# Kernel optimization log

Measured on AMD Instinct MI355X. Metric: run time of the kernel, lower is better.

## Reference

```python
import jax, jax.numpy as jnp
import numpy as np

KS = 3
N = KS ** 3  # 27 kernel taps
EPS = 1e-5

def conv3d(x, w, stride=1, padding=0):
    return jax.lax.conv_general_dilated(
        x, w, (stride,) * 3, [(padding, padding)] * 3,
        dimension_numbers=('NCDHW', 'OIDHW', 'NCDHW'))

def batchnorm(x, gamma, beta):
    mu = jnp.mean(x, axis=(0, 2, 3, 4), keepdims=True)
    var = jnp.var(x, axis=(0, 2, 3, 4), keepdims=True)
    return (x - mu) * jax.lax.rsqrt(var + EPS) * gamma[None, :, None, None, None] + beta[None, :, None, None, None]

def deform_conv3d(x, w_p, b_p, w_m, b_m, w_dc):
    b, c, D, H, W = x.shape
    offset = conv3d(x, w_p, padding=1) + b_p[None, :, None, None, None]      # (b,3N,D,H,W)
    m = jax.nn.sigmoid(conv3d(x, w_m, padding=1) + b_m[None, :, None, None, None])  # (b,N,D,H,W)
    x_pad = jnp.pad(x, ((0, 0), (0, 0), (1, 1), (1, 1), (1, 1)))
    Dp, Hp, Wp = D + 2, H + 2, W + 2
    r = jnp.arange(-(KS - 1) // 2, KS // 2 + 1, dtype=x.dtype)
    pn_d, pn_h, pn_w = [a.reshape(-1) for a in jnp.meshgrid(r, r, r, indexing='ij')]
    off = offset.transpose(0, 2, 3, 4, 1)                                    # (b,D,H,W,3N)
    p0_d = jnp.arange(1, D + 1, dtype=x.dtype)[:, None, None, None]
    p0_h = jnp.arange(1, H + 1, dtype=x.dtype)[None, :, None, None]
    p0_w = jnp.arange(1, W + 1, dtype=x.dtype)[None, None, :, None]
    pd = p0_d + pn_d + off[..., :N]
    ph = p0_h + pn_h + off[..., N:2 * N]
    pw = p0_w + pn_w + off[..., 2 * N:]
    d0 = jnp.clip(jnp.floor(pd), 0.0, Dp - 1.0); d1 = jnp.clip(d0 + 1.0, 0.0, Dp - 1.0)
    h0 = jnp.clip(jnp.floor(ph), 0.0, Hp - 1.0); h1 = jnp.clip(h0 + 1.0, 0.0, Hp - 1.0)
    w0 = jnp.clip(jnp.floor(pw), 0.0, Wp - 1.0); w1 = jnp.clip(w0 + 1.0, 0.0, Wp - 1.0)
    pd = jnp.clip(pd, 0.0, Dp - 1.0); ph = jnp.clip(ph, 0.0, Hp - 1.0); pw = jnp.clip(pw, 0.0, Wp - 1.0)
    xf = x_pad.reshape(b, c, -1)
    def gather(qd, qh, qw):
        idx = (qd * (Hp * Wp) + qh * Wp + qw).astype(jnp.int32).reshape(b, 1, -1)
        v = jnp.take_along_axis(xf, jnp.broadcast_to(idx, (b, c, idx.shape[-1])), axis=2)
        return v.reshape(b, c, D, H, W, N)
    x_off = jnp.zeros((b, c, D, H, W, N), x.dtype)
    for qd, wd in ((d0, 1.0 + d0 - pd), (d1, 1.0 - d1 + pd)):
        for qh, wh in ((h0, 1.0 + h0 - ph), (h1, 1.0 - h1 + ph)):
            for qw, ww in ((w0, 1.0 + w0 - pw), (w1, 1.0 - w1 + pw)):
                x_off = x_off + (wd * wh * ww)[:, None] * gather(qd, qh, qw)
    x_off = x_off * m.transpose(0, 2, 3, 4, 1)[:, None]                      # modulation
    # interleave kernel taps: (b,c,D,kd,H,kh,W,kw) -> (b,c,D*KS,H*KS,W*KS)
    x_off = x_off.reshape(b, c, D, H, W, KS, KS, KS)
    x_off = x_off.transpose(0, 1, 2, 5, 3, 6, 4, 7).reshape(b, c, D * KS, H * KS, W * KS)
    out = conv3d(x_off, w_dc, stride=KS)
    p = jnp.concatenate([pd, ph, pw], axis=-1)                               # (b,D,H,W,3N)
    return out, p

def setup_inputs() -> dict:
    key = jax.random.key(0)
    ks = jax.random.split(key, 10)
    B, D = 4, 48
    return {
        'x': jax.random.normal(ks[0], (B, 1, D, D, D), jnp.float32),
        'w_p': jax.random.normal(ks[1], (3 * N, 1, KS, KS, KS), jnp.float32) * 0.05,
        'b_p': jnp.zeros((3 * N,), jnp.float32),
        'w_m': jax.random.normal(ks[2], (N, 1, KS, KS, KS), jnp.float32) * 0.1,
        'b_m': jnp.zeros((N,), jnp.float32),
        'w_dc': jax.random.normal(ks[3], (1, 1, KS, KS, KS), jnp.float32) * 0.2,
        'g_d': jnp.ones((1,), jnp.float32), 'be_d': jnp.zeros((1,), jnp.float32),
        'w_c1': jax.random.normal(ks[4], (32, 1, KS, KS, KS), jnp.float32) * 0.3,
        'g1': jnp.ones((32,), jnp.float32), 'be1': jnp.zeros((32,), jnp.float32),
        'w_c2': jax.random.normal(ks[5], (64, 32, KS, KS, KS), jnp.float32) * 0.06,
        'g2': jnp.ones((64,), jnp.float32), 'be2': jnp.zeros((64,), jnp.float32),
        'w_fc': jax.random.normal(ks[6], (10, 64), jnp.float32) * 0.1,
        'b_fc': jnp.zeros((10,), jnp.float32),
    }

def reference(x, w_p, b_p, w_m, b_m, w_dc, g_d, be_d, w_c1, g1, be1, w_c2, g2, be2, w_fc, b_fc):
    inp = x
    for _ in range(2):
        y, p = deform_conv3d(inp, w_p, b_p, w_m, b_m, w_dc)
        xxx = y
        inp = jax.nn.relu(batchnorm(y, g_d, be_d))
    h = jax.nn.relu(batchnorm(conv3d(inp, w_c1, padding=1), g1, be1))
    h = jax.nn.relu(batchnorm(conv3d(h, w_c2, padding=1), g2, be2))
    h = jax.lax.reduce_window(h, -jnp.inf, jax.lax.max, (1, 1, 3, 3, 3), (1, 1, 3, 3, 3), 'VALID')
    h = h.mean(axis=(2, 3, 4))                       # adaptive avg pool to 1
    logits = h @ w_fc.T + b_fc
    return logits, xxx, p
```

## Files before the change

### kernel.cpp

```cpp
#include <hip/hip_runtime.h>
#include <math.h>

#define BSZ 4
#define DD 48
#define SS (48*48*48)
#define NV (BSZ*SS)
#define PS 125000
#define EPSBN 1e-5f

typedef __attribute__((ext_vector_type(8))) short bf16x8;
typedef __attribute__((ext_vector_type(4))) short s16x4;
typedef __attribute__((ext_vector_type(4))) float f32x4;

__device__ __forceinline__ short f2b(float f){
  unsigned u = __float_as_uint(f);
  u = (u + 0x7FFFu + ((u>>16)&1u)) >> 16;
  return (short)u;
}
__device__ __forceinline__ float b2f(short s){
  return __uint_as_float(((unsigned)(unsigned short)s)<<16);
}

__global__ __launch_bounds__(256) void pad_pair_kernel(
    const float* __restrict__ src, unsigned* __restrict__ dst)
{
  int idx = blockIdx.x*256 + threadIdx.x;
  if (idx >= BSZ*PS) return;
  int b = idx / PS; int r = idx - b*PS;
  int z = r/2500; int r2 = r - z*2500; int yy = r2/50; int xx = r2 - yy*50;
  const float* sb = src + (size_t)b*SS;
  auto val = [&](int zz,int yv,int xv)->unsigned{
    float v = 0.f;
    if (zz>=1 && zz<=48 && yv>=1 && yv<=48 && xv>=1 && xv<=48)
      v = sb[(size_t)((zz-1)*48 + (yv-1))*48 + (xv-1)];
    return (unsigned)(unsigned short)f2b(v);
  };
  unsigned lo = val(z,yy,xx);
  unsigned hi = (xx<49) ? val(z,yy,xx+1) : 0u;
  dst[idx] = lo | (hi<<16);
}

__global__ __launch_bounds__(256) void bnpad_pair_kernel(
    const float* __restrict__ y, const float* __restrict__ st,
    const float* __restrict__ gamma, const float* __restrict__ beta,
    unsigned* __restrict__ dst)
{
  int idx = blockIdx.x*256 + threadIdx.x;
  if (idx >= BSZ*PS) return;
  float mu  = st[0]*(1.f/(float)NV);
  float var = st[1]*(1.f/(float)NV) - mu*mu;
  float sc  = rsqrtf(var+EPSBN)*gamma[0];
  float sh  = beta[0] - mu*sc;
  int b = idx / PS; int r = idx - b*PS;
  int z = r/2500; int r2 = r - z*2500; int yy = r2/50; int xx = r2 - yy*50;
  const float* yb = y + (size_t)b*SS;
  auto val = [&](int zz,int yv,int xv)->unsigned{
    float v = 0.f;
    if (zz>=1 && zz<=48 && yv>=1 && yv<=48 && xv>=1 && xv<=48){
      float t = yb[(size_t)((zz-1)*48 + (yv-1))*48 + (xv-1)];
      v = fmaxf(fmaf(t, sc, sh), 0.f);
    }
    return (unsigned)(unsigned short)f2b(v);
  };
  unsigned lo = val(z,yy,xx);
  unsigned hi = (xx<49) ? val(z,yy,xx+1) : 0u;
  dst[idx] = lo | (hi<<16);
}

__global__ void repack_kernel(
    const float* __restrict__ w_c2,
    const float* __restrict__ w_p, const float* __restrict__ b_p,
    const float* __restrict__ w_m, const float* __restrict__ b_m,
    const float* __restrict__ w_c1,
    short* __restrict__ wbf, short* __restrict__ wo2, short* __restrict__ wc1b)
{
  int o = blockIdx.x*256 + threadIdx.x;
  if (o < 27*64*32){
    int ci = o & 31; int co = (o>>5) & 63; int tap = o >> 11;
    wbf[o] = f2b(w_c2[(co*32+ci)*27 + tap]);
  } else if (o < 27*64*32 + 112*32){
    int o2 = o - 27*64*32;
    int k = o2 & 31; int c = o2 >> 5;
    int f = c >> 4, qq = (c >> 2) & 3, r = c & 3;
    int n = 4*f + qq;
    float v = 0.f;
    if (n < 27){
      if (k < 27)       v = (r < 3) ? w_p[(r*27+n)*27 + k] : w_m[n*27 + k];
      else if (k == 27) v = (r < 3) ? b_p[r*27+n]          : b_m[n];
    }
    wo2[o2] = f2b(v);
  } else if (o < 27*64*32 + 112*32 + 32*32){
    int o3 = o - 27*64*32 - 112*32;
    int k = o3 & 31; int c = o3 >> 5;
    wc1b[o3] = f2b(k < 27 ? w_c1[c*27 + k] : 0.f);
  }
}

template<bool WRITE_P>
__global__ __launch_bounds__(256) void deform3_kernel(
    const unsigned* __restrict__ xpair,
    const short* __restrict__ wo2,
    const float* __restrict__ w_dc,
    float* __restrict__ y, float* __restrict__ p_out,
    float* __restrict__ st)
{
  __shared__ short xt[6*6*18];
  __shared__ __align__(16) float pbuf[WRITE_P ? 4*16*81 : 4];
  __shared__ float yred[8];

  int bid0 = blockIdx.x;
  int bid = (bid0 & 7)*216 + (bid0 >> 3);
  int bw = bid % 3; int bh = (bid/3)%12; int bd = (bid/36)%12; int b = bid/432;
  int d0 = bd*4, h0 = bh*4, w0 = bw*16;
  int tid = threadIdx.x;
  const unsigned* xp = xpair + (size_t)b*PS;

  for (int e = tid; e < 648; e += 256){
    int z = e/108; int rem = e - z*108; int yy = rem/18; int xx = rem - yy*18;
    xt[e] = (short)(xp[(d0+z)*2500 + (h0+yy)*50 + (w0+xx)] & 0xffffu);
  }
  __syncthreads();

  int lane = tid & 63, wid = tid >> 6;
  int q = lane >> 4, n16 = lane & 15;

  bf16x8 aF[7];
  #pragma unroll
  for (int f=0; f<7; ++f)
    aF[f] = *(const bf16x8*)(wo2 + (f*16 + n16)*32 + q*8);

  int toffs[8];
  #pragma unroll
  for (int j=0;j<8;++j){
    int t = q*8 + j; int tc = t > 26 ? 0 : t;
    int kd = tc/9, rr = tc - kd*9, kh = rr/3, kw = rr - kh*3;
    toffs[j] = kd*108 + kh*18 + kw;
  }

  float wdcv[7], fkd[7], fkh[7], fkw[7];
  #pragma unroll
  for (int f=0; f<7; ++f){
    int n = 4*f + q;
    if (n < 27){
      int kd = n/9, rr = n - kd*9, kh = rr/3, kw = rr - kh*3;
      wdcv[f] = w_dc[n];
      fkd[f] = (float)kd; fkh[f] = (float)kh; fkw[f] = (float)kw;
    } else { wdcv[f]=0.f; fkd[f]=0.f; fkh[f]=0.f; fkw[f]=0.f; }
  }

  const short one_bf = (short)0x3F80;
  const f32x4 zero4 = {0.f,0.f,0.f,0.f};
  float based = (float)(d0 + wid);
  float basew = (float)(w0 + n16);
  float ys = 0.f, yq = 0.f;
  float* pw = pbuf + wid*1296;

  #pragma unroll 1
  for (int dy=0; dy<4; ++dy){
    int vbase = wid*108 + dy*18 + n16;
    bf16x8 bF;
    #pragma unroll
    for (int j=0;j<8;++j){
      short xv = xt[vbase + toffs[j]];
      bF[j] = (j<3 || q<3) ? xv : one_bf;
    }
    f32x4 acc[7];
    #pragma unroll
    for (int f=0; f<7; ++f)
      acc[f] = __builtin_amdgcn_mfma_f32_16x16x32_bf16(aF[f], bF, zero4, 0,0,0);

    float baseh = (float)(h0 + dy);
    float accv = 0.f;
    #pragma unroll
    for (int f=0; f<7; ++f){
      int n = 4*f + q;
      if (n < 27){
        float od = acc[f][0], oh = acc[f][1], ow = acc[f][2], mr = acc[f][3];
        float mm = __builtin_amdgcn_rcpf(1.f + __expf(-mr));
        float pdv = based + fkd[f] + od;
        float phv = baseh + fkh[f] + oh;
        float pwv = basew + fkw[f] + ow;
        float fd0 = fminf(fmaxf(floorf(pdv),0.f),49.f), fd1 = fminf(fd0+1.f,49.f);
        float pdc = fminf(fmaxf(pdv,0.f),49.f);
        float wd0 = 1.f + fd0 - pdc, wd1 = 1.f - fd1 + pdc;
        float fh0 = fminf(fmaxf(floorf(phv),0.f),49.f), fh1 = fminf(fh0+1.f,49.f);
        float phc = fminf(fmaxf(phv,0.f),49.f);
        float wh0 = 1.f + fh0 - phc, wh1 = 1.f - fh1 + phc;
        float fw0 = fminf(fmaxf(floorf(pwv),0.f),49.f);
        float pwc = fminf(fmaxf(pwv,0.f),49.f);
        float fw1 = fminf(fw0+1.f,49.f);
        float wwa = 1.f + fw0 - pwc, wwb = 1.f - fw1 + pwc;
        int iz0 = (int)fd0*2500, iz1 = (int)fd1*2500;
        int iy0 = (int)fh0*50,   iy1 = (int)fh1*50;
        int ix0 = (int)fw0;
        bool sel = ix0 > 48;
        int ixp = sel ? 48 : ix0;
        unsigned p00 = xp[iz0+iy0+ixp], p01 = xp[iz0+iy1+ixp];
        unsigned p10 = xp[iz1+iy0+ixp], p11 = xp[iz1+iy1+ixp];
        float lo00=b2f((short)p00), hi00=b2f((short)(p00>>16));
        float lo01=b2f((short)p01), hi01=b2f((short)(p01>>16));
        float lo10=b2f((short)p10), hi10=b2f((short)(p10>>16));
        float lo11=b2f((short)p11), hi11=b2f((short)(p11>>16));
        float v000 = sel ? hi00 : lo00, v001 = hi00;
        float v010 = sel ? hi01 : lo01, v011 = hi01;
        float v100 = sel ? hi10 : lo10, v101 = hi10;
        float v110 = sel ? hi11 : lo11, v111 = hi11;
        float sv = wd0*(wh0*(wwa*v000+wwb*v001)+wh1*(wwa*v010+wwb*v011))
                 + wd1*(wh0*(wwa*v100+wwb*v101)+wh1*(wwa*v110+wwb*v111));
        accv += sv*mm*wdcv[f];
        if constexpr (WRITE_P){
          int vb = n16*81;
          pw[vb + n]      = pdc;
          pw[vb + 27 + n] = phc;
          pw[vb + 54 + n] = pwc;
        }
      }
    }
    accv += __shfl_xor(accv, 16);
    accv += __shfl_xor(accv, 32);
    if (q == 0){
      y[(size_t)b*SS + (size_t)((d0+wid)*48 + (h0+dy))*48 + (w0+n16)] = accv;
      ys += accv; yq += accv*accv;
    }

    if constexpr (WRITE_P){
      size_t rbase = ((((size_t)b*48 + (d0+wid))*48 + (h0+dy))*48 + w0)*81;
      float* dst = p_out + rbase;
      #pragma unroll
      for (int k=0;k<6;++k){
        int i = lane + (k<<6);
        if (i < 324){
          f32x4 v = *(const f32x4*)(pw + i*4);
          __builtin_nontemporal_store(v, (f32x4*)(dst + i*4));
        }
      }
    }
  }

  ys += __shfl_xor(ys, 1); ys += __shfl_xor(ys, 2);
  ys += __shfl_xor(ys, 4); ys += __shfl_xor(ys, 8);
  yq += __shfl_xor(yq, 1); yq += __shfl_xor(yq, 2);
  yq += __shfl_xor(yq, 4); yq += __shfl_xor(yq, 8);
  if (lane == 0){ yred[wid] = ys; yred[4+wid] = yq; }
  __syncthreads();
  if (tid == 0) atomicAdd(&st[0], yred[0]+yred[1]+yred[2]+yred[3]);
  if (tid == 1) atomicAdd(&st[1], yred[4]+yred[5]+yred[6]+yred[7]);
}

__global__ __launch_bounds__(256) void conv1m_kernel(
    const unsigned* __restrict__ xpair, const short* __restrict__ wc1b,
    short* __restrict__ h1c)
{
  __shared__ short xt[6*6*18];
  int bid0 = blockIdx.x;
  int bid = (bid0 & 7)*216 + (bid0 >> 3);
  int bw = bid % 3; int bh = (bid/3)%12; int bd = (bid/36)%12; int b = bid/432;
  int d0 = bd*4, h0 = bh*4, w0 = bw*16;
  int tid = threadIdx.x;
  const unsigned* xp = xpair + (size_t)b*PS;

  for (int e = tid; e < 648; e += 256){
    int z = e/108; int rem = e - z*108; int yy = rem/18; int xx = rem - yy*18;
    xt[e] = (short)(xp[(d0+z)*2500 + (h0+yy)*50 + (w0+xx)] & 0xffffu);
  }
  __syncthreads();

  int lane = tid & 63, wid = tid >> 6;
  int q = lane >> 4, n16 = lane & 15;

  bf16x8 aF0 = *(const bf16x8*)(wc1b + n16*32 + q*8);
  bf16x8 aF1 = *(const bf16x8*)(wc1b + (16+n16)*32 + q*8);

  int toffs[8];
  #pragma unroll
  for (int j=0;j<8;++j){
    int t = q*8 + j; int tc = t > 26 ? 0 : t;
    int kd = tc/9, rr = tc - kd*9, kh = rr/3, kw = rr - kh*3;
    toffs[j] = kd*108 + kh*18 + kw;
  }

  const f32x4 zero4 = {0.f,0.f,0.f,0.f};
  #pragma unroll
  for (int dy=0; dy<4; ++dy){
    int vbase = wid*108 + dy*18 + n16;
    bf16x8 bF;
    #pragma unroll
    for (int j=0;j<8;++j) bF[j] = xt[vbase + toffs[j]];
    f32x4 a0 = __builtin_amdgcn_mfma_f32_16x16x32_bf16(aF0, bF, zero4, 0,0,0);
    f32x4 a1 = __builtin_amdgcn_mfma_f32_16x16x32_bf16(aF1, bF, zero4, 0,0,0);
    size_t idx = (size_t)b*SS + (size_t)((d0+wid)*48 + (h0+dy))*48 + (w0+n16);
    s16x4 o0, o1;
    #pragma unroll
    for (int r=0;r<4;++r){ o0[r]=f2b(a0[r]); o1[r]=f2b(a1[r]); }
    *(s16x4*)(h1c + idx*32 + q*4)      = o0;
    *(s16x4*)(h1c + idx*32 + 16 + q*4) = o1;
  }
}

template<int NCH>
__global__ __launch_bounds__(256) void bn_stats_cl(
    const short* __restrict__ x, float* __restrict__ sums)
{
  constexpr int GPB = NCH/8;
  const long NG = (long)NV*GPB;
  int tid = threadIdx.x;
  f32x4 sa = {0.f,0.f,0.f,0.f}, sb = sa, qa = sa, qb = sa;
  for (long g = (long)blockIdx.x*256+tid; g < NG; g += (long)gridDim.x*256){
    bf16x8 v8 = *(const bf16x8*)(x + g*8);
    float v;
    v=b2f(v8[0]); sa[0]+=v; qa[0]+=v*v;
    v=b2f(v8[1]); sa[1]+=v; qa[1]+=v*v;
    v=b2f(v8[2]); sa[2]+=v; qa[2]+=v*v;
    v=b2f(v8[3]); sa[3]+=v; qa[3]+=v*v;
    v=b2f(v8[4]); sb[0]+=v; qb[0]+=v*v;
    v=b2f(v8[5]); sb[1]+=v; qb[1]+=v*v;
    v=b2f(v8[6]); sb[2]+=v; qb[2]+=v*v;
    v=b2f(v8[7]); sb[3]+=v; qb[3]+=v*v;
  }
  #pragma unroll
  for (int m = GPB; m < 64; m <<= 1){
    sa[0]+=__shfl_xor(sa[0],m); sa[1]+=__shfl_xor(sa[1],m);
    sa[2]+=__shfl_xor(sa[2],m); sa[3]+=__shfl_xor(sa[3],m);
    sb[0]+=__shfl_xor(sb[0],m); sb[1]+=__shfl_xor(sb[1],m);
    sb[2]+=__shfl_xor(sb[2],m); sb[3]+=__shfl_xor(sb[3],m);
    qa[0]+=__shfl_xor(qa[0],m); qa[1]+=__shfl_xor(qa[1],m);
    qa[2]+=__shfl_xor(qa[2],m); qa[3]+=__shfl_xor(qa[3],m);
    qb[0]+=__shfl_xor(qb[0],m); qb[1]+=__shfl_xor(qb[1],m);
    qb[2]+=__shfl_xor(qb[2],m); qb[3]+=__shfl_xor(qb[3],m);
  }
  int lane = tid & 63, wid = tid >> 6;
  __shared__ float red[4][GPB][16];
  if (lane < GPB){
    red[wid][lane][0]=sa[0];  red[wid][lane][1]=sa[1];
    red[wid][lane][2]=sa[2];  red[wid][lane][3]=sa[3];
    red[wid][lane][4]=sb[0];  red[wid][lane][5]=sb[1];
    red[wid][lane][6]=sb[2];  red[wid][lane][7]=sb[3];
    red[wid][lane][8]=qa[0];  red[wid][lane][9]=qa[1];
    red[wid][lane][10]=qa[2]; red[wid][lane][11]=qa[3];
    red[wid][lane][12]=qb[0]; red[wid][lane][13]=qb[1];
    red[wid][lane][14]=qb[2]; red[wid][lane][15]=qb[3];
  }
  __syncthreads();
  if (tid < GPB*16){
    int gi = tid >> 4, v = tid & 15;
    float t = red[0][gi][v] + red[1][gi][v] + red[2][gi][v] + red[3][gi][v];
    int ch = gi*8 + (v & 7);
    atomicAdd(&sums[2*ch + (v>>3)], t);
  }
}

__global__ __launch_bounds__(256) void conv2_mfma2(
    const short* __restrict__ h1c, const short* __restrict__ wbf,
    const float* __restrict__ st1, const float* __restrict__ g1,
    const float* __restrict__ be1, short* __restrict__ t2c)
{
  __shared__ __align__(16) short slab[4*648*8];
  __shared__ float ssc[32], ssh[32];
  int tid = threadIdx.x;
  if (tid < 32){
    float mu  = st1[2*tid]  *(1.f/(float)NV);
    float var = st1[2*tid+1]*(1.f/(float)NV) - mu*mu;
    float sc = rsqrtf(var+EPSBN)*g1[tid];
    ssc[tid]=sc; ssh[tid]=be1[tid]-mu*sc;
  }
  __syncthreads();

  int bid0 = blockIdx.x;
  int bid = (bid0 & 7)*216 + (bid0 >> 3);
  int bw = bid % 3; int bh = (bid/3)%12; int bd = (bid/36)%12; int b = bid/432;
  int d0 = bd*4, h0 = bh*4, w0 = bw*16;
  const short* hb = h1c + (size_t)b*SS*32;

  for (int e = tid; e < 648; e += 256){
    int z = e/108; int rem = e - z*108; int y = rem/18; int x = rem - y*18;
    int gd = d0-1+z, gh = h0-1+y, gw = w0-1+x;
    bool ok = ((unsigned)gd<48u)&&((unsigned)gh<48u)&&((unsigned)gw<48u);
    if (ok){
      const bf16x8* src = (const bf16x8*)(hb + (size_t)((gd*48+gh)*48+gw)*32);
      #pragma unroll
      for (int g8=0; g8<4; ++g8){
        bf16x8 raw = src[g8];
        bf16x8 outv;
        #pragma unroll
        for (int j=0;j<8;++j){
          float v = fmaxf(fmaf(b2f(raw[j]), ssc[g8*8+j], ssh[g8*8+j]), 0.f);
          outv[j] = f2b(v);
        }
        *(bf16x8*)&slab[(g8*648+e)*8] = outv;
      }
    } else {
      bf16x8 zz = {0,0,0,0,0,0,0,0};
      #pragma unroll
      for (int g8=0; g8<4; ++g8) *(bf16x8*)&slab[(g8*648+e)*8] = zz;
    }
  }
  __syncthreads();

  int lane = tid & 63, wid = tid >> 6;
  int q = lane >> 4, n16 = lane & 15;
  f32x4 zero4 = {0.f,0.f,0.f,0.f};
  f32x4 acc[4][4];
  #pragma unroll
  for (int i=0;i<4;++i)
  #pragma unroll
  for (int j=0;j<4;++j) acc[i][j] = zero4;

  #pragma unroll 1
  for (int tap=0; tap<27; ++tap){
    int kd = tap/9; int kh = (tap/3)%3; int kw = tap%3;
    const short* wp = wbf + (size_t)tap*64*32 + n16*32 + q*8;
    bf16x8 aF[4];
    #pragma unroll
    for (int mb=0; mb<4; ++mb)
      aF[mb] = *(const bf16x8*)(wp + mb*16*32);

    int zz = wid + kd;
    #pragma unroll
    for (int dy=0; dy<4; ++dy){
      int e = (zz*6 + (dy+kh))*18 + (n16+kw);
      bf16x8 bF = *(const bf16x8*)&slab[(q*648 + e)*8];
      #pragma unroll
      for (int mb=0; mb<4; ++mb)
        acc[mb][dy] = __builtin_amdgcn_mfma_f32_16x16x32_bf16(aF[mb], bF, acc[mb][dy], 0,0,0);
    }
  }

  short* tb = t2c + (size_t)b*SS*64;
  #pragma unroll
  for (int dy=0; dy<4; ++dy){
    int svox = ((d0+wid)*48 + (h0+dy))*48 + (w0+n16);
    #pragma unroll
    for (int mb=0; mb<4; ++mb){
      s16x4 o4;
      #pragma unroll
      for (int r=0;r<4;++r) o4[r] = f2b(acc[mb][dy][r]);
      *(s16x4*)(tb + (size_t)svox*64 + mb*16 + q*4) = o4;
    }
  }
}

__global__ __launch_bounds__(128) void pool64c_kernel(
    const short* __restrict__ t2c, const float* __restrict__ sums,
    const float* __restrict__ gamma, const float* __restrict__ beta,
    float* __restrict__ pooled)
{
  __shared__ float ssc[64], ssh[64];
  int tid = threadIdx.x;
  if (tid < 64){
    float mu  = sums[2*tid]  *(1.f/(float)NV);
    float var = sums[2*tid+1]*(1.f/(float)NV) - mu*mu;
    float sc = rsqrtf(var+EPSBN)*gamma[tid];
    ssc[tid]=sc; ssh[tid]=beta[tid]-mu*sc;
  }
  __syncthreads();
  int b = blockIdx.z, pd = blockIdx.y, ph = blockIdx.x;
  int c8 = tid & 7, pw = tid >> 3;
  const short* tb = t2c + (size_t)b*SS*64;
  f32x4 mxa = {-1e30f,-1e30f,-1e30f,-1e30f}, mxb = mxa;
  float sc0=ssc[c8*8+0], sc1=ssc[c8*8+1], sc2=ssc[c8*8+2], sc3=ssc[c8*8+3];
  float sc4=ssc[c8*8+4], sc5=ssc[c8*8+5], sc6=ssc[c8*8+6], sc7=ssc[c8*8+7];
  float sh0=ssh[c8*8+0], sh1=ssh[c8*8+1], sh2=ssh[c8*8+2], sh3=ssh[c8*8+3];
  float sh4=ssh[c8*8+4], sh5=ssh[c8*8+5], sh6=ssh[c8*8+6], sh7=ssh[c8*8+7];
  #pragma unroll
  for (int kd=0;kd<3;++kd)
  #pragma unroll 1
  for (int kh=0;kh<3;++kh)
  #pragma unroll
  for (int kw=0;kw<3;++kw){
    int vox = ((pd*3+kd)*48 + (ph*3+kh))*48 + (pw*3+kw);
    bf16x8 v8 = *(const bf16x8*)(tb + (size_t)vox*64 + c8*8);
    float v;
    v = fmaxf(fmaf(b2f(v8[0]), sc0, sh0), 0.f); mxa[0] = fmaxf(mxa[0], v);
    v = fmaxf(fmaf(b2f(v8[1]), sc1, sh1), 0.f); mxa[1] = fmaxf(mxa[1], v);
    v = fmaxf(fmaf(b2f(v8[2]), sc2, sh2), 0.f); mxa[2] = fmaxf(mxa[2], v);
    v = fmaxf(fmaf(b2f(v8[3]), sc3, sh3), 0.f); mxa[3] = fmaxf(mxa[3], v);
    v = fmaxf(fmaf(b2f(v8[4]), sc4, sh4), 0.f); mxb[0] = fmaxf(mxb[0], v);
    v = fmaxf(fmaf(b2f(v8[5]), sc5, sh5), 0.f); mxb[1] = fmaxf(mxb[1], v);
    v = fmaxf(fmaf(b2f(v8[6]), sc6, sh6), 0.f); mxb[2] = fmaxf(mxb[2], v);
    v = fmaxf(fmaf(b2f(v8[7]), sc7, sh7), 0.f); mxb[3] = fmaxf(mxb[3], v);
  }
  __shared__ float r[128][8];
  r[tid][0]=mxa[0]; r[tid][1]=mxa[1]; r[tid][2]=mxa[2]; r[tid][3]=mxa[3];
  r[tid][4]=mxb[0]; r[tid][5]=mxb[1]; r[tid][6]=mxb[2]; r[tid][7]=mxb[3];
  __syncthreads();
  for (int o=64;o>=8;o>>=1){
    if (tid<o){
      #pragma unroll
      for (int j=0;j<8;++j) r[tid][j]+=r[tid+o][j];
    }
    __syncthreads();
  }
  if (tid<8){
    #pragma unroll
    for (int j=0;j<8;++j) atomicAdd(&pooled[b*64 + tid*8 + j], r[tid][j]);
  }
}

__global__ void fc_kernel(const float* __restrict__ pooled,
                          const float* __restrict__ w_fc, const float* __restrict__ b_fc,
                          float* __restrict__ logits)
{
  int t = threadIdx.x;
  if (t < 40){
    int b = t/10, k = t - 10*(t/10);
    float a = b_fc[k];
    #pragma unroll 1
    for (int c=0;c<64;++c) a = fmaf(pooled[b*64+c]*(1.f/4096.f), w_fc[k*64+c], a);
    logits[b*10+k] = a;
  }
}

extern "C" void kernel_launch(void* const* d_in, const int* in_sizes, int n_in,
                              void* d_out, int out_size, void* d_ws, size_t ws_size,
                              hipStream_t stream)
{
  const float* x    = (const float*)d_in[0];
  const float* w_p  = (const float*)d_in[1];
  const float* b_p  = (const float*)d_in[2];
  const float* w_m  = (const float*)d_in[3];
  const float* b_m  = (const float*)d_in[4];
  const float* w_dc = (const float*)d_in[5];
  const float* g_d  = (const float*)d_in[6];
  const float* be_d = (const float*)d_in[7];
  const float* w_c1 = (const float*)d_in[8];
  const float* g1   = (const float*)d_in[9];
  const float* be1  = (const float*)d_in[10];
  const float* w_c2 = (const float*)d_in[11];
  const float* g2   = (const float*)d_in[12];
  const float* be2  = (const float*)d_in[13];
  const float* w_fc = (const float*)d_in[14];
  const float* b_fc = (const float*)d_in[15];

  float* out    = (float*)d_out;
  float* logits = out;
  float* xxx    = out + 40;
  float* p_out  = out + 40 + NV;

  float* ws     = (float*)d_ws;
  float* stats  = ws;
  float* pooled = stats + 512;
  short* wbf    = (short*)(pooled + 256);
  short* wo2    = wbf + 27*64*32;
  short* wc1b   = wo2 + 112*32;
  unsigned* xpair = (unsigned*)(wc1b + 32*32);
  float* y1     = (float*)(xpair + (size_t)BSZ*PS);
  short* h1c    = (short*)(y1 + NV);
  short* t2c    = h1c + (size_t)NV*32;

  float* st_y1 = stats + 0;
  float* st_y2 = stats + 2;
  float* st_h1 = stats + 4;
  float* st_t2 = stats + 68;

  const int pblk = (BSZ*PS + 255)/256;

  hipMemsetAsync(stats, 0, (512+256)*sizeof(float), stream);

  repack_kernel<<<(27*64*32 + 112*32 + 32*32 + 255)/256,256,0,stream>>>(
      w_c2, w_p, b_p, w_m, b_m, w_c1, wbf, wo2, wc1b);

  pad_pair_kernel<<<pblk,256,0,stream>>>(x, xpair);
  deform3_kernel<false><<<1728,256,0,stream>>>(xpair, wo2, w_dc, y1, nullptr, st_y1);
  bnpad_pair_kernel<<<pblk,256,0,stream>>>(y1, st_y1, g_d, be_d, xpair);

  deform3_kernel<true><<<1728,256,0,stream>>>(xpair, wo2, w_dc, xxx, p_out, st_y2);
  bnpad_pair_kernel<<<pblk,256,0,stream>>>(xxx, st_y2, g_d, be_d, xpair);

  conv1m_kernel<<<1728,256,0,stream>>>(xpair, wc1b, h1c);
  bn_stats_cl<32><<<256,256,0,stream>>>(h1c, st_h1);

  conv2_mfma2<<<1728,256,0,stream>>>(h1c, wbf, st_h1, g1, be1, t2c);
  bn_stats_cl<64><<<512,256,0,stream>>>(t2c, st_t2);
  pool64c_kernel<<<dim3(16,16,BSZ),128,0,stream>>>(t2c, st_t2, g2, be2, pooled);

  fc_kernel<<<1,64,0,stream>>>(pooled, w_fc, b_fc, logits);
}
```

Baseline: 330.2 us.

## Fuse BN2 statistics into pooling pass using per-window max/min

Removes the separate bn_stats pass over the 64-channel conv2 output. A single read of t2c now accumulates per-channel sum and sum of squares along with per-window max and min. A small final kernel applies the BN affine plus ReLU to the max or the min depending on the sign of the scale, then averages. This saves one full read of a large bf16 tensor, at the cost of writing a 2M-float max/min buffer into the h1c workspace region and adding one extra kernel.

```diff
diff --git a/kernel.cpp b/kernel.cpp
--- a/kernel.cpp
+++ b/kernel.cpp
@@ -439,28 +439,16 @@
   }
 }
 
-__global__ __launch_bounds__(128) void pool64c_kernel(
-    const short* __restrict__ t2c, const float* __restrict__ sums,
-    const float* __restrict__ gamma, const float* __restrict__ beta,
-    float* __restrict__ pooled)
-{
-  __shared__ float ssc[64], ssh[64];
+__global__ __launch_bounds__(128) void pool_stats_kernel(
+    const short* __restrict__ t2c, float* __restrict__ wmm, float* __restrict__ st2)
+{
   int tid = threadIdx.x;
-  if (tid < 64){
-    float mu  = sums[2*tid]  *(1.f/(float)NV);
-    float var = sums[2*tid+1]*(1.f/(float)NV) - mu*mu;
-    float sc = rsqrtf(var+EPSBN)*gamma[tid];
-    ssc[tid]=sc; ssh[tid]=beta[tid]-mu*sc;
-  }
-  __syncthreads();
   int b = blockIdx.z, pd = blockIdx.y, ph = blockIdx.x;
   int c8 = tid & 7, pw = tid >> 3;
   const short* tb = t2c + (size_t)b*SS*64;
   f32x4 mxa = {-1e30f,-1e30f,-1e30f,-1e30f}, mxb = mxa;
-  float sc0=ssc[c8*8+0], sc1=ssc[c8*8+1], sc2=ssc[c8*8+2], sc3=ssc[c8*8+3];
-  float sc4=ssc[c8*8+4], sc5=ssc[c8*8+5], sc6=ssc[c8*8+6], sc7=ssc[c8*8+7];
-  float sh0=ssh[c8*8+0], sh1=ssh[c8*8+1], sh2=ssh[c8*8+2], sh3=ssh[c8*8+3];
-  float sh4=ssh[c8*8+4], sh5=ssh[c8*8+5], sh6=ssh[c8*8+6], sh7=ssh[c8*8+7];
+  f32x4 mna = { 1e30f, 1e30f, 1e30f, 1e30f}, mnb = mna;
+  f32x4 sa = {0.f,0.f,0.f,0.f}, sb = sa, qa = sa, qb = sa;
   #pragma unroll
   for (int kd=0;kd<3;++kd)
   #pragma unroll 1
@@ -470,30 +458,71 @@
     int vox = ((pd*3+kd)*48 + (ph*3+kh))*48 + (pw*3+kw);
     bf16x8 v8 = *(const bf16x8*)(tb + (size_t)vox*64 + c8*8);
     float v;
-    v = fmaxf(fmaf(b2f(v8[0]), sc0, sh0), 0.f); mxa[0] = fmaxf(mxa[0], v);
-    v = fmaxf(fmaf(b2f(v8[1]), sc1, sh1), 0.f); mxa[1] = fmaxf(mxa[1], v);
-    v = fmaxf(fmaf(b2f(v8[2]), sc2, sh2), 0.f); mxa[2] = fmaxf(mxa[2], v);
-    v = fmaxf(fmaf(b2f(v8[3]), sc3, sh3), 0.f); mxa[3] = fmaxf(mxa[3], v);
-    v = fmaxf(fmaf(b2f(v8[4]), sc4, sh4), 0.f); mxb[0] = fmaxf(mxb[0], v);
-    v = fmaxf(fmaf(b2f(v8[5]), sc5, sh5), 0.f); mxb[1] = fmaxf(mxb[1], v);
-    v = fmaxf(fmaf(b2f(v8[6]), sc6, sh6), 0.f); mxb[2] = fmaxf(mxb[2], v);
-    v = fmaxf(fmaf(b2f(v8[7]), sc7, sh7), 0.f); mxb[3] = fmaxf(mxb[3], v);
-  }
-  __shared__ float r[128][8];
-  r[tid][0]=mxa[0]; r[tid][1]=mxa[1]; r[tid][2]=mxa[2]; r[tid][3]=mxa[3];
-  r[tid][4]=mxb[0]; r[tid][5]=mxb[1]; r[tid][6]=mxb[2]; r[tid][7]=mxb[3];
+    v=b2f(v8[0]); mxa[0]=fmaxf(mxa[0],v); mna[0]=fminf(mna[0],v); sa[0]+=v; qa[0]+=v*v;
+    v=b2f(v8[1]); mxa[1]=fmaxf(mxa[1],v); mna[1]=fminf(mna[1],v); sa[1]+=v; qa[1]+=v*v;
+    v=b2f(v8[2]); mxa[2]=fmaxf(mxa[2],v); mna[2]=fminf(mna[2],v); sa[2]+=v; qa[2]+=v*v;
+    v=b2f(v8[3]); mxa[3]=fmaxf(mxa[3],v); mna[3]=fminf(mna[3],v); sa[3]+=v; qa[3]+=v*v;
+    v=b2f(v8[4]); mxb[0]=fmaxf(mxb[0],v); mnb[0]=fminf(mnb[0],v); sb[0]+=v; qb[0]+=v*v;
+    v=b2f(v8[5]); mxb[1]=fmaxf(mxb[1],v); mnb[1]=fminf(mnb[1],v); sb[1]+=v; qb[1]+=v*v;
+    v=b2f(v8[6]); mxb[2]=fmaxf(mxb[2],v); mnb[2]=fminf(mnb[2],v); sb[2]+=v; qb[2]+=v*v;
+    v=b2f(v8[7]); mxb[3]=fmaxf(mxb[3],v); mnb[3]=fminf(mnb[3],v); sb[3]+=v; qb[3]+=v*v;
+  }
+  int wloc = ((pd*16 + ph)<<4) + pw;
+  int base0 = (c8*8)*16384 + b*4096 + wloc;
+  #pragma unroll
+  for (int j=0;j<4;++j){
+    wmm[base0 + j*16384]            = mxa[j];
+    wmm[base0 + (4+j)*16384]        = mxb[j];
+    wmm[1048576 + base0 + j*16384]     = mna[j];
+    wmm[1048576 + base0 + (4+j)*16384] = mnb[j];
+  }
+  __shared__ float r[128][16];
+  #pragma unroll
+  for (int j=0;j<4;++j){
+    r[tid][j]    = sa[j]; r[tid][4+j]  = sb[j];
+    r[tid][8+j]  = qa[j]; r[tid][12+j] = qb[j];
+  }
   __syncthreads();
   for (int o=64;o>=8;o>>=1){
     if (tid<o){
       #pragma unroll
-      for (int j=0;j<8;++j) r[tid][j]+=r[tid+o][j];
+      for (int k=0;k<16;++k) r[tid][k]+=r[tid+o][k];
     }
     __syncthreads();
   }
   if (tid<8){
     #pragma unroll
-    for (int j=0;j<8;++j) atomicAdd(&pooled[b*64 + tid*8 + j], r[tid][j]);
-  }
+    for (int j=0;j<8;++j){
+      atomicAdd(&st2[2*(tid*8+j)],   r[tid][j]);
+      atomicAdd(&st2[2*(tid*8+j)+1], r[tid][8+j]);
+    }
+  }
+}
+
+__global__ __launch_bounds__(256) void pool_final_kernel(
+    const float* __restrict__ wmm, const float* __restrict__ st2,
+    const float* __restrict__ gamma, const float* __restrict__ beta,
+    float* __restrict__ pooled)
+{
+  int bid = blockIdx.x;
+  int b = bid >> 6, c = bid & 63;
+  float mu  = st2[2*c]  *(1.f/(float)NV);
+  float var = st2[2*c+1]*(1.f/(float)NV) - mu*mu;
+  float sc  = rsqrtf(var+EPSBN)*gamma[c];
+  float sh  = beta[c] - mu*sc;
+  const float* base = wmm + (sc >= 0.f ? 0 : 1048576) + c*16384 + b*4096;
+  int tid = threadIdx.x;
+  float s = 0.f;
+  #pragma unroll
+  for (int k=0;k<16;++k)
+    s += fmaxf(fmaf(base[tid + (k<<8)], sc, sh), 0.f);
+  __shared__ float r[256];
+  r[tid] = s; __syncthreads();
+  for (int o=128;o>0;o>>=1){
+    if (tid<o) r[tid]+=r[tid+o];
+    __syncthreads();
+  }
+  if (tid==0) pooled[b*64+c] = r[0];
 }
 
 __global__ void fc_kernel(const float* __restrict__ pooled,
@@ -546,6 +575,7 @@
   float* y1     = (float*)(xpair + (size_t)BSZ*PS);
   short* h1c    = (short*)(y1 + NV);
   short* t2c    = h1c + (size_t)NV*32;
+  float* wmm    = (float*)h1c;
 
   float* st_y1 = stats + 0;
   float* st_y2 = stats + 2;
@@ -554,7 +584,7 @@
 
   const int pblk = (BSZ*PS + 255)/256;
 
-  hipMemsetAsync(stats, 0, (512+256)*sizeof(float), stream);
+  hipMemsetAsync(stats, 0, 512*sizeof(float), stream);
 
   repack_kernel<<<(27*64*32 + 112*32 + 32*32 + 255)/256,256,0,stream>>>(
       w_c2, w_p, b_p, w_m, b_m, w_c1, wbf, wo2, wc1b);
@@ -570,8 +600,9 @@
   bn_stats_cl<32><<<256,256,0,stream>>>(h1c, st_h1);
 
   conv2_mfma2<<<1728,256,0,stream>>>(h1c, wbf, st_h1, g1, be1, t2c);
-  bn_stats_cl<64><<<512,256,0,stream>>>(t2c, st_t2);
-  pool64c_kernel<<<dim3(16,16,BSZ),128,0,stream>>>(t2c, st_t2, g2, be2, pooled);
+
+  pool_stats_kernel<<<dim3(16,16,BSZ),128,0,stream>>>(t2c, wmm, st_t2);
+  pool_final_kernel<<<256,256,0,stream>>>(wmm, st_t2, g2, be2, pooled);
 
   fc_kernel<<<1,64,0,stream>>>(pooled, w_fc, b_fc, logits);
 }
```

New measurement: 654.6 us. +98.3%, slower.
